# Kernel tuning notes

Measured on AMD Instinct MI355X. Metric: run time of the kernel, lower is better.

The kernel has to match this reference:

```python
import jax, jax.numpy as jnp
import numpy as np

D_MODEL = 768
NHEAD = 12
D_K = D_MODEL // NHEAD
D_FF = 3072
EPS = 1e-6


def layer_norm(x, a, b):
    # torch LayerNorm here: mean/std over last dim, std is UNBIASED (n-1), eps added to std
    n = x.shape[-1]
    m = jnp.mean(x, axis=-1, keepdims=True)
    var = jnp.sum((x - m) ** 2, axis=-1, keepdims=True) / (n - 1)
    return a * (x - m) / (jnp.sqrt(var) + EPS) + b


def setup_inputs() -> dict:
    key = jax.random.key(0)
    ks = jax.random.split(key, 12)
    B, S = 2, 2048
    s = 1.0 / np.sqrt(D_MODEL)
    inp = {
        'x': jax.random.normal(ks[0], (B, S, D_MODEL), jnp.float32),
        'mask': jnp.ones((B, 1, S), jnp.int32),
        'Wq': jax.random.normal(ks[1], (D_MODEL, D_MODEL), jnp.float32) * s,
        'bq': jnp.zeros((D_MODEL,), jnp.float32),
        'Wk': jax.random.normal(ks[2], (D_MODEL, D_MODEL), jnp.float32) * s,
        'bk': jnp.zeros((D_MODEL,), jnp.float32),
        'Wv': jax.random.normal(ks[3], (D_MODEL, D_MODEL), jnp.float32) * s,
        'bv': jnp.zeros((D_MODEL,), jnp.float32),
        'Wo': jax.random.normal(ks[4], (D_MODEL, D_MODEL), jnp.float32) * s,
        'bo': jnp.zeros((D_MODEL,), jnp.float32),
        'ln1_a': jnp.ones((D_MODEL,), jnp.float32),
        'ln1_b': jnp.zeros((D_MODEL,), jnp.float32),
        'W1': jax.random.normal(ks[5], (D_MODEL, D_FF), jnp.float32) * s,
        'b1': jnp.zeros((D_FF,), jnp.float32),
        'W2': jax.random.normal(ks[6], (D_FF, D_MODEL), jnp.float32) * (1.0 / np.sqrt(D_FF)),
        'b2': jnp.zeros((D_MODEL,), jnp.float32),
        'ln2_a': jnp.ones((D_MODEL,), jnp.float32),
        'ln2_b': jnp.zeros((D_MODEL,), jnp.float32),
    }
    return inp


def reference(x, mask, Wq, bq, Wk, bk, Wv, bv, Wo, bo, ln1_a, ln1_b, W1, b1, W2, b2, ln2_a, ln2_b):
    B, S, _ = x.shape
    # --- sublayer 1: pre-norm self-attention + residual (dropout = eval/no-op) ---
    h = layer_norm(x, ln1_a, ln1_b)
    q = (h @ Wq + bq).reshape(B, S, NHEAD, D_K).transpose(0, 2, 1, 3)  # [B,H,S,Dk]
    k = (h @ Wk + bk).reshape(B, S, NHEAD, D_K).transpose(0, 2, 1, 3)
    v = (h @ Wv + bv).reshape(B, S, NHEAD, D_K).transpose(0, 2, 1, 3)
    scores = jnp.einsum('bhqd,bhkd->bhqk', q, k) / np.sqrt(D_K)  # [B,H,S,S]
    scores = jnp.where(mask[:, None] == 0, jnp.float32(-1e9), scores)
    attn = jax.nn.softmax(scores, axis=-1)
    ctx = jnp.einsum('bhqk,bhkd->bhqd', attn, v)  # [B,H,S,Dk]
    ctx = ctx.transpose(0, 2, 1, 3).reshape(B, S, D_MODEL)
    x = x + (ctx @ Wo + bo)
    # --- sublayer 2: pre-norm FFN + residual ---
    h2 = layer_norm(x, ln2_a, ln2_b)
    ff = jax.nn.relu(h2 @ W1 + b1) @ W2 + b2
    return x + ff
```

## Files before the change

### kernel.cpp

```cpp
#include <hip/hip_runtime.h>
#include <hip/hip_bf16.h>
#include <stdint.h>

#define DM 768
#define DFF 3072
#define NH 12
#define DK 64
#define SS 2048
#define NTOK 4096
#define KCH 2

typedef __hip_bfloat16 bf16;
typedef short bf16x8 __attribute__((ext_vector_type(8)));
typedef float f32x4 __attribute__((ext_vector_type(4)));

#define MFMA16(a, b, c) __builtin_amdgcn_mfma_f32_16x16x32_bf16((a), (b), (c), 0, 0, 0)

#define QSCALE 0.18033688011112042f

#if __has_builtin(__builtin_amdgcn_exp2f)
#define EXP2F(x) __builtin_amdgcn_exp2f(x)
#else
#define EXP2F(x) exp2f(x)
#endif

static __device__ __forceinline__ bf16 f2b(float f) { return __float2bfloat16(f); }
static __device__ __forceinline__ unsigned short f2b_bits(float f) {
    bf16 h = __float2bfloat16(f);
    return *reinterpret_cast<unsigned short*>(&h);
}
static __device__ __forceinline__ float b2f(bf16 h) { return __bfloat162float(h); }

static __device__ __forceinline__ void g2l16(const void* g, void* l) {
    __builtin_amdgcn_global_load_lds(
        (const __attribute__((address_space(1))) unsigned int*)g,
        (__attribute__((address_space(3))) unsigned int*)(uintptr_t)l,
        16, 0, 0);
}

__global__ __launch_bounds__(256) void transpose_all(const float* Wq, const float* Wk,
                                                     const float* Wv, const float* Wo,
                                                     const float* W1, const float* W2,
                                                     bf16* WqT, bf16* WkT, bf16* WvT,
                                                     bf16* WoT, bf16* W1T, bf16* W2T) {
    __shared__ float tile[32][33];
    int id = blockIdx.x;
    const float* W; bf16* WT; int K, N, n0, k0;
    if (id < 2304) {
        int z = id / 576, r = id % 576;
        W  = (z == 0) ? Wq : (z == 1) ? Wk : (z == 2) ? Wv : Wo;
        WT = (z == 0) ? WqT : (z == 1) ? WkT : (z == 2) ? WvT : WoT;
        K = 768; N = 768; n0 = (r % 24) * 32; k0 = (r / 24) * 32;
    } else if (id < 4608) {
        int r = id - 2304; W = W1; WT = W1T;
        K = 768; N = 3072; n0 = (r % 96) * 32; k0 = (r / 96) * 32;
    } else {
        int r = id - 4608; W = W2; WT = W2T;
        K = 3072; N = 768; n0 = (r % 24) * 32; k0 = (r / 24) * 32;
    }
    int tx = threadIdx.x & 31, ty = threadIdx.x >> 5;
#pragma unroll
    for (int r = ty; r < 32; r += 8)
        tile[r][tx] = W[(size_t)(k0 + r) * N + n0 + tx];
    __syncthreads();
#pragma unroll
    for (int r = ty; r < 32; r += 8)
        WT[(size_t)(n0 + r) * K + k0 + tx] = f2b(tile[tx][r]);
}

__global__ __launch_bounds__(256) void ln_fwd(const float* __restrict__ x,
                                              const float* __restrict__ g,
                                              const float* __restrict__ be,
                                              bf16* __restrict__ out) {
    int wid = threadIdx.x >> 6, lane = threadIdx.x & 63;
    int row = blockIdx.x * 4 + wid;
    const float* xr = x + (size_t)row * DM;
    float v[12];
    float s = 0.f;
#pragma unroll
    for (int i = 0; i < 12; ++i) { v[i] = xr[lane + i * 64]; s += v[i]; }
#pragma unroll
    for (int off = 32; off >= 1; off >>= 1) s += __shfl_xor(s, off);
    float mean = s * (1.f / 768.f);
    float s2 = 0.f;
#pragma unroll
    for (int i = 0; i < 12; ++i) { float d = v[i] - mean; s2 += d * d; }
#pragma unroll
    for (int off = 32; off >= 1; off >>= 1) s2 += __shfl_xor(s2, off);
    float rstd = 1.f / (sqrtf(s2 * (1.f / 767.f)) + 1e-6f);
    bf16* orow = out + (size_t)row * DM;
#pragma unroll
    for (int i = 0; i < 12; ++i) {
        int c = lane + i * 64;
        orow[c] = f2b(g[c] * (v[i] - mean) * rstd + be[c]);
    }
}

__device__ __forceinline__ void gemm_core(const bf16* __restrict__ A,
                                          const bf16* __restrict__ BT,
                                          int K, int bm, int bn,
                                          bf16* As, bf16* Bs,
                                          f32x4 acc[4][4]) {
    int tid = threadIdx.x;
    int lane = tid & 63, quad = lane >> 4, lid = lane & 15;
    int wid = tid >> 6;
    int wm = (wid >> 1) * 64, wn = (wid & 1) * 64;
    int s0 = tid, s1 = tid + 256;
    int r0 = s0 >> 2, c0 = (s0 & 3) ^ ((r0 >> 1) & 3);
    int r1 = s1 >> 2, c1 = (s1 & 3) ^ ((r1 >> 1) & 3);
    const bf16* A0 = A + (size_t)(bm + r0) * K + c0 * 8;
    const bf16* A1 = A + (size_t)(bm + r1) * K + c1 * 8;
    const bf16* B0 = BT + (size_t)(bn + r0) * K + c0 * 8;
    const bf16* B1 = BT + (size_t)(bn + r1) * K + c1 * 8;
    int rdc = quad ^ ((lid >> 1) & 3);
    g2l16(A0, As + s0 * 8);
    g2l16(B0, Bs + s0 * 8);
    g2l16(A1, As + s1 * 8);
    g2l16(B1, Bs + s1 * 8);
    for (int k0 = 0; k0 < K; k0 += 32) {
        __syncthreads();
        int cur = (k0 >> 5) & 1;
        if (k0 + 32 < K) {
            int nb = (cur ^ 1) * 4096;
            g2l16(A0 + k0 + 32, As + nb + s0 * 8);
            g2l16(B0 + k0 + 32, Bs + nb + s0 * 8);
            g2l16(A1 + k0 + 32, As + nb + s1 * 8);
            g2l16(B1 + k0 + 32, Bs + nb + s1 * 8);
        }
        const bf16* Ac = As + cur * 4096;
        const bf16* Bc = Bs + cur * 4096;
        bf16x8 af[4], bfr[4];
#pragma unroll
        for (int i = 0; i < 4; ++i) af[i]  = *(const bf16x8*)&Ac[(wm + i * 16 + lid) * 32 + rdc * 8];
#pragma unroll
        for (int j = 0; j < 4; ++j) bfr[j] = *(const bf16x8*)&Bc[(wn + j * 16 + lid) * 32 + rdc * 8];
#pragma unroll
        for (int i = 0; i < 4; ++i)
#pragma unroll
            for (int j = 0; j < 4; ++j)
                acc[i][j] = MFMA16(af[i], bfr[j], acc[i][j]);
    }
}

__global__ __launch_bounds__(256) void gemm_qkv(const bf16* __restrict__ A,
                                                const bf16* __restrict__ WqT,
                                                const bf16* __restrict__ WkT,
                                                const bf16* __restrict__ WvT,
                                                const float* __restrict__ bq,
                                                const float* __restrict__ bk,
                                                const float* __restrict__ bv,
                                                bf16* __restrict__ qb,
                                                bf16* __restrict__ kb,
                                                bf16* __restrict__ vtb) {
    __shared__ bf16 As[2 * 128 * 32];
    __shared__ bf16 Bs[2 * 128 * 32];
    int which = blockIdx.x / 6;
    int bn = (blockIdx.x % 6) * 128;
    int bm = blockIdx.y * 128;
    const bf16* BT = (which == 0) ? WqT : (which == 1) ? WkT : WvT;
    const float* bias = (which == 0) ? bq : (which == 1) ? bk : bv;
    f32x4 acc[4][4] = {};
    gemm_core(A, BT, DM, bm, bn, As, Bs, acc);

    int tid = threadIdx.x, wid = tid >> 6, lane = tid & 63, quad = lane >> 4, lid = lane & 15;
    int wm = (wid >> 1) * 64, wn = (wid & 1) * 64;
    float sc = (which == 0) ? QSCALE : 1.f;
#pragma unroll
    for (int j = 0; j < 4; ++j) {
        int col = bn + wn + j * 16 + lid;
        float bb = bias[col];
        int hh = col >> 6, d = col & 63;
#pragma unroll
        for (int i = 0; i < 4; ++i) {
            int rowbase = bm + wm + i * 16 + quad * 4;
            int b = rowbase >> 11;
            int s0 = rowbase & 2047;
            if (which == 2) {
                ushort4 pk;
                pk.x = f2b_bits(acc[i][j][0] + bb);
                pk.y = f2b_bits(acc[i][j][1] + bb);
                pk.z = f2b_bits(acc[i][j][2] + bb);
                pk.w = f2b_bits(acc[i][j][3] + bb);
                *(ushort4*)&vtb[(((size_t)b * NH + hh) * DK + d) * SS + s0] = pk;
            } else {
                bf16* dst = which ? kb : qb;
#pragma unroll
                for (int r = 0; r < 4; ++r)
                    dst[(((size_t)b * NH + hh) * SS + (s0 + r)) * DK + d] = f2b((acc[i][j][r] + bb) * sc);
            }
        }
    }
}

template <int EPI>
__global__ __launch_bounds__(256) void gemm_ep(const bf16* __restrict__ A,
                                               const bf16* __restrict__ BT,
                                               const float* __restrict__ bias,
                                               const float* __restrict__ res,
                                               void* __restrict__ outp,
                                               int N, int K) {
    __shared__ bf16 As[2 * 128 * 32];
    __shared__ bf16 Bs[2 * 128 * 32];
    int bm = blockIdx.y * 128, bn = blockIdx.x * 128;
    f32x4 acc[4][4] = {};
    gemm_core(A, BT, K, bm, bn, As, Bs, acc);

    int tid = threadIdx.x, wid = tid >> 6, lane = tid & 63, quad = lane >> 4, lid = lane & 15;
    int wm = (wid >> 1) * 64, wn = (wid & 1) * 64;
#pragma unroll
    for (int j = 0; j < 4; ++j) {
        int col = bn + wn + j * 16 + lid;
        float bb = bias[col];
#pragma unroll
        for (int i = 0; i < 4; ++i) {
#pragma unroll
            for (int r = 0; r < 4; ++r) {
                int row = bm + wm + i * 16 + quad * 4 + r;
                float v = acc[i][j][r] + bb;
                if (EPI == 2) {
                    ((float*)outp)[(size_t)row * N + col] = res[(size_t)row * N + col] + v;
                } else {
                    ((bf16*)outp)[(size_t)row * N + col] = f2b(fmaxf(v, 0.f));
                }
            }
        }
    }
}

template <int EPI>
__global__ __launch_bounds__(512) void gemm_ep64(const bf16* __restrict__ A,
                                                 const bf16* __restrict__ BT,
                                                 const float* __restrict__ bias,
                                                 const float* __restrict__ res,
                                                 void* __restrict__ outp,
                                                 int N, int K) {
    __shared__ char smem[49152];
    int tid = threadIdx.x;
    int half = tid >> 8, htid = tid & 255;
    bf16* As = (bf16*)smem + half * 4096;
    bf16* Bs = (bf16*)(smem + 16384) + half * 8192;
    int K2 = K >> 1, koff = half * K2;
    int bm = blockIdx.y * 64, bn = blockIdx.x * 128;
    int wid = htid >> 6, lane = tid & 63, quad = lane >> 4, lid = lane & 15;
    int wm = (wid >> 1) * 32, wn = (wid & 1) * 64;
    f32x4 acc[2][4] = {};
    int ra = htid >> 2, ca = (htid & 3) ^ ((ra >> 1) & 3);
    int s0 = htid, s1 = htid + 256;
    int rb0 = s0 >> 2, cb0 = (s0 & 3) ^ ((rb0 >> 1) & 3);
    int rb1 = s1 >> 2, cb1 = (s1 & 3) ^ ((rb1 >> 1) & 3);
    const bf16* Ap = A + (size_t)(bm + ra) * K + koff + ca * 8;
    const bf16* B0 = BT + (size_t)(bn + rb0) * K + koff + cb0 * 8;
    const bf16* B1 = BT + (size_t)(bn + rb1) * K + koff + cb1 * 8;
    int rdc = quad ^ ((lid >> 1) & 3);
    g2l16(Ap, As + htid * 8);
    g2l16(B0, Bs + s0 * 8);
    g2l16(B1, Bs + s1 * 8);
    for (int k0 = 0; k0 < K2; k0 += 32) {
        __syncthreads();
        int cur = (k0 >> 5) & 1;
        if (k0 + 32 < K2) {
            g2l16(Ap + k0 + 32, As + (cur ^ 1) * 2048 + htid * 8);
            g2l16(B0 + k0 + 32, Bs + (cur ^ 1) * 4096 + s0 * 8);
            g2l16(B1 + k0 + 32, Bs + (cur ^ 1) * 4096 + s1 * 8);
        }
        const bf16* Ac = As + cur * 2048;
        const bf16* Bc = Bs + cur * 4096;
        bf16x8 af[2], bfr[4];
#pragma unroll
        for (int i = 0; i < 2; ++i) af[i]  = *(const bf16x8*)&Ac[(wm + i * 16 + lid) * 32 + rdc * 8];
#pragma unroll
        for (int j = 0; j < 4; ++j) bfr[j] = *(const bf16x8*)&Bc[(wn + j * 16 + lid) * 32 + rdc * 8];
#pragma unroll
        for (int i = 0; i < 2; ++i)
#pragma unroll
            for (int j = 0; j < 4; ++j)
                acc[i][j] = MFMA16(af[i], bfr[j], acc[i][j]);
    }
    __syncthreads();
    float* red = (float*)smem;
    if (half == 1) {
#pragma unroll
        for (int i = 0; i < 2; ++i)
#pragma unroll
            for (int j = 0; j < 4; ++j) {
                int c = i * 4 + j;
                *(f32x4*)&red[htid * 32 + ((c ^ (htid & 7)) << 2)] = acc[i][j];
            }
    }
    __syncthreads();
    if (half == 0) {
#pragma unroll
        for (int i = 0; i < 2; ++i)
#pragma unroll
            for (int j = 0; j < 4; ++j) {
                int c = i * 4 + j;
                f32x4 o = *(const f32x4*)&red[htid * 32 + ((c ^ (htid & 7)) << 2)];
                acc[i][j] += o;
            }
#pragma unroll
        for (int j = 0; j < 4; ++j) {
            int col = bn + wn + j * 16 + lid;
            float bb = bias[col];
#pragma unroll
            for (int i = 0; i < 2; ++i) {
#pragma unroll
                for (int r = 0; r < 4; ++r) {
                    int row = bm + wm + i * 16 + quad * 4 + r;
                    float v = acc[i][j][r] + bb;
                    if (EPI == 2) {
                        ((float*)outp)[(size_t)row * N + col] = res[(size_t)row * N + col] + v;
                    } else {
                        ((bf16*)outp)[(size_t)row * N + col] = f2b(fmaxf(v, 0.f));
                    }
                }
            }
        }
    }
}

__global__ __launch_bounds__(256) void attn_part(const bf16* __restrict__ qb,
                                                 const bf16* __restrict__ kb,
                                                 const bf16* __restrict__ vtb,
                                                 const int* __restrict__ mask,
                                                 bf16* __restrict__ part,
                                                 float* __restrict__ lws) {
    __shared__ bf16 Ks[2 * 64 * 64];
    __shared__ bf16 VTs[2 * 64 * 64];
    __shared__ bf16 Ps[128 * 72];
    int bh = blockIdx.y;
    int b = bh / NH;
    int q0 = blockIdx.x * 128;
    int kc = blockIdx.z;
    const bf16* Kp = kb  + (size_t)bh * SS * DK;
    const bf16* VT = vtb + (size_t)bh * DK * SS;
    int tid = threadIdx.x, wid = tid >> 6, lane = tid & 63, quad = lane >> 4, lid = lane & 15;

    int s0 = tid, s1 = tid + 256;
    int r0 = s0 >> 3, c0 = (s0 & 7) ^ (r0 & 7);
    int r1 = s1 >> 3, c1 = (s1 & 7) ^ (r1 & 7);

    bf16x8 qf0[2], qf1[2];
#pragma unroll
    for (int u = 0; u < 2; ++u) {
        const bf16* Qrow = qb + ((size_t)bh * SS + q0 + wid * 32 + u * 16 + lid) * DK;
        qf0[u] = *(const bf16x8*)&Qrow[quad * 8];
        qf1[u] = *(const bf16x8*)&Qrow[32 + quad * 8];
    }

    bf16x8 ones;
#pragma unroll
    for (int i = 0; i < 8; ++i) ones[i] = (short)0x3F80;

    int rdc  = quad ^ (lid & 7);
    int rdc2 = rdc ^ 4;
    const int* mrow = mask + b * SS;

    f32x4 accv[2][4] = {};
    f32x4 accl[2] = {};

    int tbeg = kc * (SS / 64 / KCH), tend = (kc + 1) * (SS / 64 / KCH);

    {
        int k0 = tbeg * 64;
        g2l16(Kp + (size_t)(k0 + r0) * DK + c0 * 8, Ks + s0 * 8);
        g2l16(Kp + (size_t)(k0 + r1) * DK + c1 * 8, Ks + s1 * 8);
        g2l16(VT + (size_t)r0 * SS + k0 + c0 * 8, VTs + s0 * 8);
        g2l16(VT + (size_t)r1 * SS + k0 + c1 * 8, VTs + s1 * 8);
    }

    int cur = 0;
    for (int t = tbeg; t < tend; ++t) {
        int k0 = t * 64;
        __syncthreads();
        if (t + 1 < tend) {
            int k0n = (t + 1) * 64;
            int nb = (cur ^ 1) * 4096;
            g2l16(Kp + (size_t)(k0n + r0) * DK + c0 * 8, Ks + nb + s0 * 8);
            g2l16(Kp + (size_t)(k0n + r1) * DK + c1 * 8, Ks + nb + s1 * 8);
            g2l16(VT + (size_t)r0 * SS + k0n + c0 * 8, VTs + nb + s0 * 8);
            g2l16(VT + (size_t)r1 * SS + k0n + c1 * 8, VTs + nb + s1 * 8);
        }
        const bf16* Kc  = Ks  + cur * 4096;
        const bf16* VTc = VTs + cur * 4096;

#pragma unroll
        for (int ns = 0; ns < 4; ++ns) {
            bf16x8 kf0 = *(const bf16x8*)&Kc[(ns * 16 + lid) * 64 + rdc * 8];
            bf16x8 kf1 = *(const bf16x8*)&Kc[(ns * 16 + lid) * 64 + rdc2 * 8];
            int4 mk = *(const int4*)&mrow[k0 + ns * 16 + quad * 4];
#pragma unroll
            for (int u = 0; u < 2; ++u) {
                f32x4 st = {};
                st = MFMA16(kf0, qf0[u], st);
                st = MFMA16(kf1, qf1[u], st);
                float p0 = mk.x ? EXP2F(st[0]) : 0.f;
                float p1 = mk.y ? EXP2F(st[1]) : 0.f;
                float p2 = mk.z ? EXP2F(st[2]) : 0.f;
                float p3 = mk.w ? EXP2F(st[3]) : 0.f;
                __hip_bfloat162 h01 = __float22bfloat162_rn(make_float2(p0, p1));
                __hip_bfloat162 h23 = __float22bfloat162_rn(make_float2(p2, p3));
                uint2 pw;
                pw.x = *(unsigned int*)&h01;
                pw.y = *(unsigned int*)&h23;
                *(uint2*)&Ps[(wid * 32 + u * 16 + lid) * 72 + ns * 16 + quad * 4] = pw;
            }
        }

        bf16x8 pa0[2], pa1[2];
#pragma unroll
        for (int u = 0; u < 2; ++u) {
            pa0[u] = *(const bf16x8*)&Ps[(wid * 32 + u * 16 + lid) * 72 + quad * 8];
            pa1[u] = *(const bf16x8*)&Ps[(wid * 32 + u * 16 + lid) * 72 + 32 + quad * 8];
            accl[u] = MFMA16(pa0[u], ones, accl[u]);
            accl[u] = MFMA16(pa1[u], ones, accl[u]);
        }

#pragma unroll
        for (int ds = 0; ds < 4; ++ds) {
            bf16x8 vf0 = *(const bf16x8*)&VTc[(ds * 16 + lid) * 64 + rdc * 8];
            bf16x8 vf1 = *(const bf16x8*)&VTc[(ds * 16 + lid) * 64 + rdc2 * 8];
#pragma unroll
            for (int u = 0; u < 2; ++u) {
                accv[u][ds] = MFMA16(pa0[u], vf0, accv[u][ds]);
                accv[u][ds] = MFMA16(pa1[u], vf1, accv[u][ds]);
            }
        }
        cur ^= 1;
    }

    bf16* pb = part + ((size_t)kc * (2 * NH) + bh) * DK * SS;
#pragma unroll
    for (int u = 0; u < 2; ++u) {
        if (lid == 0) {
#pragma unroll
            for (int r = 0; r < 4; ++r)
                lws[((size_t)kc * (2 * NH) + bh) * SS + q0 + wid * 32 + u * 16 + quad * 4 + r] = accl[u][r];
        }
        int qbase = q0 + wid * 32 + u * 16 + quad * 4;
#pragma unroll
        for (int ds = 0; ds < 4; ++ds) {
            int d = ds * 16 + lid;
            ushort4 pk;
            pk.x = f2b_bits(accv[u][ds][0]);
            pk.y = f2b_bits(accv[u][ds][1]);
            pk.z = f2b_bits(accv[u][ds][2]);
            pk.w = f2b_bits(accv[u][ds][3]);
            *(ushort4*)&pb[(size_t)d * SS + qbase] = pk;
        }
    }
}

__global__ __launch_bounds__(256) void attn_combine(const bf16* __restrict__ part,
                                                    const float* __restrict__ lws,
                                                    bf16* __restrict__ ctx) {
    __shared__ float tile[64][66];
    __shared__ float linv[64];
    int bh = blockIdx.y;
    int b = bh / NH, h = bh % NH;
    int q0 = blockIdx.x * 64;
    int tid = threadIdx.x;

    if (tid < 64) {
        float l = 0.f;
#pragma unroll
        for (int kc = 0; kc < KCH; ++kc)
            l += lws[((size_t)kc * (2 * NH) + bh) * SS + q0 + tid];
        linv[tid] = 1.f / l;
    }

    int d = tid >> 2, qs = (tid & 3) * 16;
    const bf16* p0 = part + (((size_t)0 * (2 * NH) + bh) * DK + d) * SS + q0 + qs;
    const bf16* p1 = part + (((size_t)1 * (2 * NH) + bh) * DK + d) * SS + q0 + qs;
    bf16x8 a0 = *(const bf16x8*)p0;
    bf16x8 a1 = *(const bf16x8*)(p0 + 8);
    bf16x8 b0 = *(const bf16x8*)p1;
    bf16x8 b1 = *(const bf16x8*)(p1 + 8);
#pragma unroll
    for (int i = 0; i < 8; ++i) {
        tile[d][qs + i]     = b2f(((const bf16*)&a0)[i]) + b2f(((const bf16*)&b0)[i]);
        tile[d][qs + 8 + i] = b2f(((const bf16*)&a1)[i]) + b2f(((const bf16*)&b1)[i]);
    }
    __syncthreads();

    int q = tid >> 2, ds2 = (tid & 3) * 16;
    float rl = linv[q];
    unsigned int wv[8];
#pragma unroll
    for (int i = 0; i < 8; ++i) {
        __hip_bfloat162 hh = __float22bfloat162_rn(
            make_float2(tile[ds2 + 2 * i][q] * rl, tile[ds2 + 2 * i + 1][q] * rl));
        wv[i] = *(unsigned int*)&hh;
    }
    bf16* crow = ctx + (size_t)(b * SS + q0 + q) * DM + h * DK + ds2;
    uint4 u0 = {wv[0], wv[1], wv[2], wv[3]};
    uint4 u1 = {wv[4], wv[5], wv[6], wv[7]};
    *(uint4*)&crow[0] = u0;
    *(uint4*)&crow[8] = u1;
}

extern "C" void kernel_launch(void* const* d_in, const int* in_sizes, int n_in,
                              void* d_out, int out_size, void* d_ws, size_t ws_size,
                              hipStream_t stream) {
    const float* x    = (const float*)d_in[0];
    const int*   mask = (const int*)d_in[1];
    const float* Wq   = (const float*)d_in[2];
    const float* bq   = (const float*)d_in[3];
    const float* Wk   = (const float*)d_in[4];
    const float* bk   = (const float*)d_in[5];
    const float* Wv   = (const float*)d_in[6];
    const float* bv   = (const float*)d_in[7];
    const float* Wo   = (const float*)d_in[8];
    const float* bo   = (const float*)d_in[9];
    const float* ln1a = (const float*)d_in[10];
    const float* ln1b = (const float*)d_in[11];
    const float* W1   = (const float*)d_in[12];
    const float* b1   = (const float*)d_in[13];
    const float* W2   = (const float*)d_in[14];
    const float* b2   = (const float*)d_in[15];
    const float* ln2a = (const float*)d_in[16];
    const float* ln2b = (const float*)d_in[17];
    float* out = (float*)d_out;

    char* w = (char*)d_ws;
    bf16* h   = (bf16*)w; w += (size_t)NTOK * DM * 2;
    bf16* qb  = (bf16*)w; w += (size_t)NTOK * DM * 2;
    bf16* kb  = (bf16*)w; w += (size_t)NTOK * DM * 2;
    bf16* vtb = (bf16*)w; w += (size_t)NTOK * DM * 2;
    bf16* ctx = (bf16*)w; w += (size_t)NTOK * DM * 2;
    bf16* h2  = (bf16*)w; w += (size_t)NTOK * DM * 2;
    bf16* ffa = (bf16*)w; w += (size_t)NTOK * DFF * 2;
    float* x1 = (float*)w; w += (size_t)NTOK * DM * 4;
    bf16* WqT = (bf16*)w; w += (size_t)DM * DM * 2;
    bf16* WkT = (bf16*)w; w += (size_t)DM * DM * 2;
    bf16* WvT = (bf16*)w; w += (size_t)DM * DM * 2;
    bf16* WoT = (bf16*)w; w += (size_t)DM * DM * 2;
    bf16* W1T = (bf16*)w; w += (size_t)DM * DFF * 2;
    bf16* W2T = (bf16*)w; w += (size_t)DM * DFF * 2;

    bf16*  part = ffa;
    float* lws  = x1;

    transpose_all<<<6912, 256, 0, stream>>>(Wq, Wk, Wv, Wo, W1, W2,
                                            WqT, WkT, WvT, WoT, W1T, W2T);

    ln_fwd<<<NTOK / 4, 256, 0, stream>>>(x, ln1a, ln1b, h);
    gemm_qkv<<<dim3(18, 32), 256, 0, stream>>>(h, WqT, WkT, WvT, bq, bk, bv, qb, kb, vtb);
    attn_part<<<dim3(SS / 128, 2 * NH, KCH), 256, 0, stream>>>(qb, kb, vtb, mask, part, lws);
    attn_combine<<<dim3(SS / 64, 2 * NH), 256, 0, stream>>>(part, lws, ctx);
    gemm_ep64<2><<<dim3(6, 64), 512, 0, stream>>>(ctx, WoT, bo, x, (void*)x1, DM, DM);
    ln_fwd<<<NTOK / 4, 256, 0, stream>>>(x1, ln2a, ln2b, h2);
    gemm_ep<3><<<dim3(24, 32), 256, 0, stream>>>(h2, W1T, b1, nullptr, (void*)ffa, DFF, DM);
    gemm_ep64<2><<<dim3(6, 64), 512, 0, stream>>>(ffa, W2T, b2, x1, (void*)out, DM, DFF);
}
```

Baseline: 288.2 us.

## Triple-buffer gemm_ep64 LDS pipeline with explicit vmcnt waits

Changes the split-K 64x128 GEMM (used for the Wo and W2 projections with residual epilogue) from double to triple buffering. Two tiles are prefetched ahead and explicit s_waitcnt vmcnt plus raw s_barrier replace __syncthreads, so global-to-LDS loads overlap more MFMA work. LDS use grows from 48KB to 72KB per block, which may reduce occupancy.

```diff
diff --git a/kernel.cpp b/kernel.cpp
--- a/kernel.cpp
+++ b/kernel.cpp
@@ -23,6 +23,9 @@
 #else
 #define EXP2F(x) exp2f(x)
 #endif
+
+#define ASM_VMCNT3 asm volatile("s_waitcnt vmcnt(3)" ::: "memory")
+#define ASM_VMCNT0 asm volatile("s_waitcnt vmcnt(0)" ::: "memory")
 
 static __device__ __forceinline__ bf16 f2b(float f) { return __float2bfloat16(f); }
 static __device__ __forceinline__ unsigned short f2b_bits(float f) {
@@ -234,12 +237,13 @@
                                                  const float* __restrict__ res,
                                                  void* __restrict__ outp,
                                                  int N, int K) {
-    __shared__ char smem[49152];
+    __shared__ char smem[73728];
     int tid = threadIdx.x;
     int half = tid >> 8, htid = tid & 255;
-    bf16* As = (bf16*)smem + half * 4096;
-    bf16* Bs = (bf16*)(smem + 16384) + half * 8192;
+    bf16* As = (bf16*)smem + half * 6144;
+    bf16* Bs = (bf16*)(smem + 24576) + half * 12288;
     int K2 = K >> 1, koff = half * K2;
+    int nt = K2 >> 5;
     int bm = blockIdx.y * 64, bn = blockIdx.x * 128;
     int wid = htid >> 6, lane = tid & 63, quad = lane >> 4, lid = lane & 15;
     int wm = (wid >> 1) * 32, wn = (wid & 1) * 64;
@@ -252,19 +256,29 @@
     const bf16* B0 = BT + (size_t)(bn + rb0) * K + koff + cb0 * 8;
     const bf16* B1 = BT + (size_t)(bn + rb1) * K + koff + cb1 * 8;
     int rdc = quad ^ ((lid >> 1) & 3);
-    g2l16(Ap, As + htid * 8);
-    g2l16(B0, Bs + s0 * 8);
-    g2l16(B1, Bs + s1 * 8);
-    for (int k0 = 0; k0 < K2; k0 += 32) {
-        __syncthreads();
-        int cur = (k0 >> 5) & 1;
-        if (k0 + 32 < K2) {
-            g2l16(Ap + k0 + 32, As + (cur ^ 1) * 2048 + htid * 8);
-            g2l16(B0 + k0 + 32, Bs + (cur ^ 1) * 4096 + s0 * 8);
-            g2l16(B1 + k0 + 32, Bs + (cur ^ 1) * 4096 + s1 * 8);
-        }
-        const bf16* Ac = As + cur * 2048;
-        const bf16* Bc = Bs + cur * 4096;
+
+    g2l16(Ap,      As + htid * 8);
+    g2l16(B0,      Bs + s0 * 8);
+    g2l16(B1,      Bs + s1 * 8);
+    g2l16(Ap + 32, As + 2048 + htid * 8);
+    g2l16(B0 + 32, Bs + 4096 + s0 * 8);
+    g2l16(B1 + 32, Bs + 4096 + s1 * 8);
+
+    int bcur = 0;
+    for (int t = 0; t < nt; ++t) {
+        __builtin_amdgcn_sched_barrier(0);
+        if (t + 1 < nt) { ASM_VMCNT3; } else { ASM_VMCNT0; }
+        __builtin_amdgcn_s_barrier();
+        __builtin_amdgcn_sched_barrier(0);
+        if (t + 2 < nt) {
+            int bi = bcur >= 1 ? bcur - 1 : 2;
+            int ko = (t + 2) * 32;
+            g2l16(Ap + ko, As + bi * 2048 + htid * 8);
+            g2l16(B0 + ko, Bs + bi * 4096 + s0 * 8);
+            g2l16(B1 + ko, Bs + bi * 4096 + s1 * 8);
+        }
+        const bf16* Ac = As + bcur * 2048;
+        const bf16* Bc = Bs + bcur * 4096;
         bf16x8 af[2], bfr[4];
 #pragma unroll
         for (int i = 0; i < 2; ++i) af[i]  = *(const bf16x8*)&Ac[(wm + i * 16 + lid) * 32 + rdc * 8];
@@ -275,6 +289,7 @@
 #pragma unroll
             for (int j = 0; j < 4; ++j)
                 acc[i][j] = MFMA16(af[i], bfr[j], acc[i][j]);
+        bcur = bcur < 2 ? bcur + 1 : 0;
     }
     __syncthreads();
     float* red = (float*)smem;
```

Measured after the change: 292.8 us. No clear change (+1.6%).
